# Kernel tuning notes

Hardware: AMD Instinct MI355X
Metric: run time of the kernel (lower is better)

## Reference

```python
import jax, jax.numpy as jnp
import numpy as np

N = 4_194_304  # rays
D = 8          # depth values per ray
IGNORE_VALUE = 0.0  # config.multiDepthIgnoreValue[net_idx]


def setup_inputs() -> dict:
    key = jax.random.key(0)
    k1, k2 = jax.random.split(key)
    outputs = jax.random.normal(k1, (N, D), dtype=jnp.float32)
    targets = jax.random.uniform(k2, (N, D), dtype=jnp.float32)
    return {"outputs": outputs, "targets": targets}


def reference(outputs, targets):
    n, d = outputs.shape
    rows = jnp.arange(n)
    big = jnp.finfo(outputs.dtype).max

    # Sequential greedy matching: for each target column i, find the closest
    # remaining output per row, record its index, and knock it out with +inf.
    def step(out_cpy, t_col):
        # out_cpy: [N, D], t_col: [N]
        ids = jnp.argmin(jnp.abs(out_cpy - t_col[:, None]), axis=-1)  # [N]
        out_cpy = out_cpy.at[rows, ids].set(big)
        return out_cpy, ids

    _, ids_all = jax.lax.scan(step, outputs, targets.T)  # ids_all: [D, N]
    resort_indices = ids_all.T  # [N, D]

    outputs_shfled = jnp.take_along_axis(outputs, resort_indices, axis=1)
    # targets.data / outputs_shfled.data -> stop_gradient semantics for seltargets
    seltargets = jnp.where(targets != IGNORE_VALUE, targets,
                           jax.lax.stop_gradient(outputs_shfled))
    return jnp.mean((outputs_shfled - seltargets) ** 2)
```

## Files before the change

kernel.cpp:

```cpp
#include <hip/hip_runtime.h>
#include <cfloat>


#define DVALS 8

__global__ __launch_bounds__(256) void mdmse_match_kernel(
    const float* __restrict__ outputs,
    const float* __restrict__ targets,
    float* __restrict__ accum,
    int n_rows)
{
    int tid = blockIdx.x * blockDim.x + threadIdx.x;
    int stride = gridDim.x * blockDim.x;

    float local = 0.0f;

    for (int row = tid; row < n_rows; row += stride) {
        const float4* op = reinterpret_cast<const float4*>(outputs + (size_t)row * DVALS);
        const float4* tp = reinterpret_cast<const float4*>(targets + (size_t)row * DVALS);
        float4 o0 = op[0], o1 = op[1];
        float4 t0 = tp[0], t1 = tp[1];

        float o[DVALS] = {o0.x, o0.y, o0.z, o0.w, o1.x, o1.y, o1.z, o1.w};
        float t[DVALS] = {t0.x, t0.y, t0.z, t0.w, t1.x, t1.y, t1.z, t1.w};

        float cpy[DVALS];
#pragma unroll
        for (int j = 0; j < DVALS; ++j) cpy[j] = o[j];

#pragma unroll
        for (int i = 0; i < DVALS; ++i) {
            float tc = t[i];
            float bd = FLT_MAX;
            int bi = -1;
#pragma unroll
            for (int j = 0; j < DVALS; ++j) {
                float d = fabsf(cpy[j] - tc);
                bool better = d < bd;
                bd = better ? d : bd;
                bi = better ? j : bi;
            }
            float bestv = 0.0f;
#pragma unroll
            for (int j = 0; j < DVALS; ++j) {
                bool hit = (bi == j);
                bestv = hit ? cpy[j] : bestv;
                cpy[j] = hit ? FLT_MAX : cpy[j];
            }
            float diff = (tc != 0.0f) ? (bestv - tc) : 0.0f;
            local = fmaf(diff, diff, local);
        }
    }

#pragma unroll
    for (int off = 32; off > 0; off >>= 1)
        local += __shfl_down(local, off, 64);

    __shared__ float wsum[4];
    int lane = threadIdx.x & 63;
    int wid  = threadIdx.x >> 6;
    if (lane == 0) wsum[wid] = local;
    __syncthreads();

    if (threadIdx.x == 0) {
        float s = wsum[0] + wsum[1] + wsum[2] + wsum[3];
        atomicAdd(accum, s);
    }
}

__global__ void mdmse_finalize_kernel(const float* __restrict__ accum,
                                      float* __restrict__ out,
                                      float inv_count)
{
    out[0] = accum[0] * inv_count;
}

extern "C" void kernel_launch(void* const* d_in, const int* in_sizes, int n_in,
                              void* d_out, int out_size, void* d_ws, size_t ws_size,
                              hipStream_t stream)
{
    const float* outputs = (const float*)d_in[0];
    const float* targets = (const float*)d_in[1];
    float* out = (float*)d_out;
    float* accum = (float*)d_ws;

    const int n_rows = in_sizes[0] / DVALS;

    hipMemsetAsync(accum, 0, sizeof(float), stream);

    const int block = 256;
    int grid = 2048;
    int max_grid = (n_rows + block - 1) / block;
    if (grid > max_grid) grid = max_grid;

    mdmse_match_kernel<<<grid, block, 0, stream>>>(outputs, targets, accum, n_rows);

    const float inv_count = 1.0f / ((float)n_rows * (float)DVALS);
    mdmse_finalize_kernel<<<1, 1, 0, stream>>>(accum, out, inv_count);
}
```

Baseline: 281.4 us.

## Batch four rows per thread, drop finalize kernel, and use distance as diff

Each thread now loads four rows up front before doing the greedy matching, so more memory loads are in flight per thread. The grid is sized so each thread handles about four rows instead of using a fixed 2048 blocks. The best distance is reused as the squared-error term in place of gathering the selected value, and the finalize kernel is removed by scaling each block's partial sum before the atomic add into the output. The costs are higher register use, many more atomics on a single address from the larger grid, and a final sum that now depends on atomic ordering.

```diff
diff --git a/kernel.cpp b/kernel.cpp
--- a/kernel.cpp
+++ b/kernel.cpp
@@ -3,52 +3,63 @@
 
 
 #define DVALS 8
+#define ROWS_PER_THREAD 4
 
 __global__ __launch_bounds__(256) void mdmse_match_kernel(
     const float* __restrict__ outputs,
     const float* __restrict__ targets,
-    float* __restrict__ accum,
-    int n_rows)
+    float* __restrict__ out,
+    int n_rows,
+    float inv_count)
 {
     int tid = blockIdx.x * blockDim.x + threadIdx.x;
     int stride = gridDim.x * blockDim.x;
 
     float local = 0.0f;
 
-    for (int row = tid; row < n_rows; row += stride) {
-        const float4* op = reinterpret_cast<const float4*>(outputs + (size_t)row * DVALS);
-        const float4* tp = reinterpret_cast<const float4*>(targets + (size_t)row * DVALS);
-        float4 o0 = op[0], o1 = op[1];
-        float4 t0 = tp[0], t1 = tp[1];
-
-        float o[DVALS] = {o0.x, o0.y, o0.z, o0.w, o1.x, o1.y, o1.z, o1.w};
-        float t[DVALS] = {t0.x, t0.y, t0.z, t0.w, t1.x, t1.y, t1.z, t1.w};
-
-        float cpy[DVALS];
+    for (int base = tid; base < n_rows; base += stride * ROWS_PER_THREAD) {
+        float4 ov[ROWS_PER_THREAD][2];
+        float4 tv4[ROWS_PER_THREAD][2];
+        bool valid[ROWS_PER_THREAD];
 #pragma unroll
-        for (int j = 0; j < DVALS; ++j) cpy[j] = o[j];
+        for (int k = 0; k < ROWS_PER_THREAD; ++k) {
+            int r = base + k * stride;
+            valid[k] = (r < n_rows);
+            if (valid[k]) {
+                const float4* op = reinterpret_cast<const float4*>(outputs + (size_t)r * DVALS);
+                const float4* tp = reinterpret_cast<const float4*>(targets + (size_t)r * DVALS);
+                ov[k][0] = op[0]; ov[k][1] = op[1];
+                tv4[k][0] = tp[0]; tv4[k][1] = tp[1];
+            }
+        }
 
 #pragma unroll
-        for (int i = 0; i < DVALS; ++i) {
-            float tc = t[i];
-            float bd = FLT_MAX;
-            int bi = -1;
+        for (int k = 0; k < ROWS_PER_THREAD; ++k) {
+            if (!valid[k]) continue;
+            float cpy[DVALS] = {ov[k][0].x, ov[k][0].y, ov[k][0].z, ov[k][0].w,
+                                ov[k][1].x, ov[k][1].y, ov[k][1].z, ov[k][1].w};
+            float t[DVALS]   = {tv4[k][0].x, tv4[k][0].y, tv4[k][0].z, tv4[k][0].w,
+                                tv4[k][1].x, tv4[k][1].y, tv4[k][1].z, tv4[k][1].w};
+
 #pragma unroll
-            for (int j = 0; j < DVALS; ++j) {
-                float d = fabsf(cpy[j] - tc);
-                bool better = d < bd;
-                bd = better ? d : bd;
-                bi = better ? j : bi;
+            for (int i = 0; i < DVALS; ++i) {
+                float tc = t[i];
+                float bd = FLT_MAX;
+                int bi = -1;
+#pragma unroll
+                for (int j = 0; j < DVALS; ++j) {
+                    float d = fabsf(cpy[j] - tc);
+                    bool better = d < bd;
+                    bd = better ? d : bd;
+                    bi = better ? j : bi;
+                }
+#pragma unroll
+                for (int j = 0; j < DVALS; ++j)
+                    cpy[j] = (bi == j) ? FLT_MAX : cpy[j];
+
+                float c = (tc != 0.0f) ? bd : 0.0f;
+                local = fmaf(c, c, local);
             }
-            float bestv = 0.0f;
-#pragma unroll
-            for (int j = 0; j < DVALS; ++j) {
-                bool hit = (bi == j);
-                bestv = hit ? cpy[j] : bestv;
-                cpy[j] = hit ? FLT_MAX : cpy[j];
-            }
-            float diff = (tc != 0.0f) ? (bestv - tc) : 0.0f;
-            local = fmaf(diff, diff, local);
         }
     }
 
@@ -64,15 +75,8 @@
 
     if (threadIdx.x == 0) {
         float s = wsum[0] + wsum[1] + wsum[2] + wsum[3];
-        atomicAdd(accum, s);
+        atomicAdd(out, s * inv_count);
     }
-}
-
-__global__ void mdmse_finalize_kernel(const float* __restrict__ accum,
-                                      float* __restrict__ out,
-                                      float inv_count)
-{
-    out[0] = accum[0] * inv_count;
 }
 
 extern "C" void kernel_launch(void* const* d_in, const int* in_sizes, int n_in,
@@ -82,19 +86,18 @@
     const float* outputs = (const float*)d_in[0];
     const float* targets = (const float*)d_in[1];
     float* out = (float*)d_out;
-    float* accum = (float*)d_ws;
 
     const int n_rows = in_sizes[0] / DVALS;
 
-    hipMemsetAsync(accum, 0, sizeof(float), stream);
+    hipMemsetAsync(out, 0, sizeof(float), stream);
 
     const int block = 256;
-    int grid = 2048;
-    int max_grid = (n_rows + block - 1) / block;
-    if (grid > max_grid) grid = max_grid;
-
-    mdmse_match_kernel<<<grid, block, 0, stream>>>(outputs, targets, accum, n_rows);
+    long long want = ((long long)n_rows + block * ROWS_PER_THREAD - 1) /
+                     (block * ROWS_PER_THREAD);
+    int grid = (int)want;
+    if (grid < 1) grid = 1;
 
     const float inv_count = 1.0f / ((float)n_rows * (float)DVALS);
-    mdmse_finalize_kernel<<<1, 1, 0, stream>>>(accum, out, inv_count);
+    mdmse_match_kernel<<<grid, block, 0, stream>>>(outputs, targets, out,
+                                                   n_rows, inv_count);
 }
```

Result: no change. 280.8 us (-0.2%).
